# Performance work log

Hardware: AMD Instinct MI355X
Metric: run time of the kernel (lower is better)

Reference implementation:

```python
import jax, jax.numpy as jnp
import numpy as np

ENC_HID = 512
DEC_HID = 512


def setup_inputs() -> dict:
    key = jax.random.key(0)
    k1, k2, k3, k4, k5 = jax.random.split(key, 5)
    hidden = jax.random.normal(k1, (64, DEC_HID), dtype=jnp.float32)
    encoder_outputs = jax.random.normal(k2, (1024, 64, 2 * ENC_HID), dtype=jnp.float32)
    in_dim = 2 * ENC_HID + DEC_HID
    # Linear params (stored as [in, out] for x @ W + b)
    scale = 1.0 / np.sqrt(in_dim)
    W = jax.random.uniform(k3, (in_dim, DEC_HID), dtype=jnp.float32, minval=-scale, maxval=scale)
    b = jax.random.uniform(k4, (DEC_HID,), dtype=jnp.float32, minval=-scale, maxval=scale)
    v = jax.random.uniform(k5, (DEC_HID,), dtype=jnp.float32)  # torch.rand in [0,1)
    return {"hidden": hidden, "encoder_outputs": encoder_outputs, "W": W, "b": b, "v": v}


def reference(hidden, encoder_outputs, W, b, v):
    # hidden: [B, Dd]; encoder_outputs: [S, B, 2*De]
    src_len = encoder_outputs.shape[0]
    enc = jnp.transpose(encoder_outputs, (1, 0, 2))            # [B, S, 2*De]
    hid = jnp.broadcast_to(hidden[:, None, :], (hidden.shape[0], src_len, hidden.shape[1]))  # [B, S, Dd]
    concat = jnp.concatenate([hid, enc], axis=2)               # [B, S, Dd+2*De]
    energy = jnp.tanh(concat @ W + b)                          # [B, S, Dd]
    scores = jnp.einsum("bsd,d->bs", energy, v)                # [B, S]
    return jax.nn.softmax(scores, axis=1)
```

## Files before the change

kernel.cpp:

```cpp
#include <hip/hip_runtime.h>
#include <stdint.h>


typedef float  floatx4 __attribute__((ext_vector_type(4)));
typedef float  floatx8 __attribute__((ext_vector_type(8)));
typedef __bf16 bf16x8  __attribute__((ext_vector_type(8)));
typedef short  short8  __attribute__((ext_vector_type(8)));

union bfu { bf16x8 v; short8 s; };

#define LOG2E_X2 2.8853900817779268f

__device__ __forceinline__ void async_ld16(const void* g, void* l) {
  __builtin_amdgcn_global_load_lds(
      (const __attribute__((address_space(1))) void*)g,
      (__attribute__((address_space(3))) void*)l, 16, 0, 0);
}

__global__ void wt_convert(const float* __restrict__ W, __bf16* __restrict__ Wt) {
  __shared__ float tile[64][65];
  const int kt = blockIdx.x >> 3;
  const int nt = blockIdx.x & 7;
  const int c  = threadIdx.x & 63;
  const int r4 = threadIdx.x >> 6;
  #pragma unroll 4
  for (int i = 0; i < 16; i++) {
    int r = i * 4 + r4;
    tile[r][c] = W[(long)(512 + kt * 64 + r) * 512 + nt * 64 + c];
  }
  __syncthreads();
  #pragma unroll 4
  for (int i = 0; i < 16; i++) {
    int n = i * 4 + r4;
    Wt[(long)(nt * 64 + n) * 1024 + kt * 64 + c] = (__bf16)tile[c][n];
  }
}

__global__ void hproj_kernel(const float* __restrict__ hidden,
                             const float* __restrict__ W,
                             const float* __restrict__ bias,
                             float* __restrict__ hproj) {
  const int tid = threadIdx.x;
  const int b_  = blockIdx.x >> 2;
  const int kc  = blockIdx.x & 3;
  __shared__ float hid[128];
  if (tid < 128) hid[tid] = hidden[b_ * 512 + kc * 128 + tid];
  __syncthreads();
  float acc = (kc == 0) ? bias[tid] : 0.f;
  const float* Wp = W + (long)(kc * 128) * 512 + tid;
  #pragma unroll 8
  for (int k = 0; k < 128; k++) acc = fmaf(hid[k], Wp[(long)k * 512], acc);
  atomicAdd(&hproj[b_ * 512 + tid], acc);
}

__global__ __launch_bounds__(256, 2) void gemm_score(
    const float* __restrict__ enc,
    const __bf16* __restrict__ Wt,
    const float* __restrict__ hproj,
    const float* __restrict__ v,
    float* __restrict__ scores)
{
  __shared__ float ldsA0[2048];
  __shared__ float ldsA1[2048];
  __shared__ float bscore[64];

  const int tid  = threadIdx.x;
  const int lane = tid & 63;
  const int wv   = tid >> 6;
  const int q    = lane >> 4;
  const int t    = lane & 15;
  const long m0  = (long)blockIdx.x * 64;

  const __bf16* bp = Wt + (long)(wv * 128 + t) * 1024 + q * 8;

  if (tid < 64) bscore[tid] = 0.f;

  floatx4 acc[4][8];
  #pragma unroll
  for (int i = 0; i < 4; i++)
    #pragma unroll
    for (int j = 0; j < 8; j++)
      acc[i][j] = (floatx4){0.f, 0.f, 0.f, 0.f};

  auto issueA = [&](int kk, float* buf) {
    #pragma unroll
    for (int i = 0; i < 2; i++) {
      int idx = i * 256 + tid;
      int c = idx >> 7, m = (idx >> 1) & 63, h = idx & 1;
      async_ld16(enc + (m0 + m) * 1024 + kk + c * 8 + h * 4, buf + idx * 4);
    }
  };
  auto loadB = [&](int kk, short8* br) {
    #pragma unroll
    for (int ct = 0; ct < 8; ct++) {
      union bfu u;
      u.v = *(const bf16x8*)(bp + kk + ct * 16 * 1024);
      br[ct] = u.s;
    }
  };
  auto fragA = [&](const float* buf, short8* af) {
    #pragma unroll
    for (int rt = 0; rt < 4; rt++) {
      floatx8 av = *(const floatx8*)(buf + (q * 128 + (rt * 16 + t) * 2) * 4);
      union bfu u;
      #pragma unroll
      for (int j = 0; j < 8; j++) u.v[j] = (__bf16)av[j];
      af[rt] = u.s;
    }
  };
  auto domfma = [&](short8* af, short8* br) {
    #pragma unroll
    for (int rt = 0; rt < 4; rt++)
      #pragma unroll
      for (int ct = 0; ct < 8; ct++)
        acc[rt][ct] = __builtin_amdgcn_mfma_f32_16x16x32_bf16(
            af[rt], br[ct], acc[rt][ct], 0, 0, 0);
  };

  short8 b0[8], b1[8], afr[4];

  issueA(0, ldsA0);
  loadB(0, b0);
  __syncthreads();

  for (int T = 0; T < 16; T++) {
    const int kk = T * 64;
    issueA(kk + 32, ldsA1);
    loadB(kk + 32, b1);
    fragA(ldsA0, afr);
    domfma(afr, b0);
    __syncthreads();

    if (T < 15) {
      issueA(kk + 64, ldsA0);
      loadB(kk + 64, b0);
    }
    fragA(ldsA1, afr);
    domfma(afr, b1);
    __syncthreads();
  }

  float vv[8];
  #pragma unroll
  for (int ct = 0; ct < 8; ct++) vv[ct] = v[wv * 128 + ct * 16 + t];

  #pragma unroll
  for (int rt = 0; rt < 4; rt++) {
    #pragma unroll
    for (int r = 0; r < 4; r++) {
      int row = rt * 16 + q * 4 + r;
      const float* hrow = hproj + row * 512 + wv * 128 + t;
      float s = 0.f;
      #pragma unroll
      for (int ct = 0; ct < 8; ct++) {
        float e  = acc[rt][ct][r] + hrow[ct * 16];
        float ex = __builtin_amdgcn_exp2f(e * LOG2E_X2);
        float th = 1.f - 2.f * __builtin_amdgcn_rcpf(ex + 1.f);
        s = fmaf(vv[ct], th, s);
      }
      s += __shfl_xor(s, 1);
      s += __shfl_xor(s, 2);
      s += __shfl_xor(s, 4);
      s += __shfl_xor(s, 8);
      if (t == 0) atomicAdd(&bscore[row], s);
    }
  }
  __syncthreads();
  if (tid < 64) scores[(long)tid * 1024 + blockIdx.x] = bscore[tid];
}

__global__ void softmax_kernel(const float* __restrict__ scores,
                               float* __restrict__ out) {
  const int b_   = blockIdx.x;
  const int tid  = threadIdx.x;
  const int lane = tid & 63;
  const int wv   = tid >> 6;
  __shared__ float redmax[4], redsum[4];

  float x[4];
  #pragma unroll
  for (int i = 0; i < 4; i++) x[i] = scores[b_ * 1024 + i * 256 + tid];
  float mx = fmaxf(fmaxf(x[0], x[1]), fmaxf(x[2], x[3]));
  #pragma unroll
  for (int off = 1; off < 64; off <<= 1) mx = fmaxf(mx, __shfl_xor(mx, off));
  if (lane == 0) redmax[wv] = mx;
  __syncthreads();
  mx = fmaxf(fmaxf(redmax[0], redmax[1]), fmaxf(redmax[2], redmax[3]));

  float e[4], s = 0.f;
  #pragma unroll
  for (int i = 0; i < 4; i++) { e[i] = __expf(x[i] - mx); s += e[i]; }
  #pragma unroll
  for (int off = 1; off < 64; off <<= 1) s += __shfl_xor(s, off);
  if (lane == 0) redsum[wv] = s;
  __syncthreads();
  s = redsum[0] + redsum[1] + redsum[2] + redsum[3];
  float inv = 1.f / s;
  #pragma unroll
  for (int i = 0; i < 4; i++) out[b_ * 1024 + i * 256 + tid] = e[i] * inv;
}

extern "C" void kernel_launch(void* const* d_in, const int* in_sizes, int n_in,
                              void* d_out, int out_size, void* d_ws, size_t ws_size,
                              hipStream_t stream) {
  (void)in_sizes; (void)n_in; (void)out_size; (void)ws_size;
  const float* hidden = (const float*)d_in[0];
  const float* enc    = (const float*)d_in[1];
  const float* W      = (const float*)d_in[2];
  const float* bias   = (const float*)d_in[3];
  const float* v      = (const float*)d_in[4];
  float* out = (float*)d_out;

  char* ws = (char*)d_ws;
  __bf16* Wt    = (__bf16*)ws;
  float*  hproj = (float*)(ws + (1 << 20));
  float*  scores= (float*)(ws + (1 << 20) + (128 << 10));

  hipMemsetAsync(hproj, 0, 64 * 512 * sizeof(float), stream);
  wt_convert<<<128, 256, 0, stream>>>(W, Wt);
  hproj_kernel<<<256, 512, 0, stream>>>(hidden, W, bias, hproj);
  gemm_score<<<1024, 256, 0, stream>>>(enc, Wt, hproj, v, scores);
  softmax_kernel<<<64, 256, 0, stream>>>(scores, out);
}
```

Measured before the change: 493.0 us.

## Stage encoder tiles through registers as bf16 with deeper software pipeline

```diff
diff --git a/kernel.cpp b/kernel.cpp
--- a/kernel.cpp
+++ b/kernel.cpp
@@ -3,19 +3,12 @@
 
 
 typedef float  floatx4 __attribute__((ext_vector_type(4)));
-typedef float  floatx8 __attribute__((ext_vector_type(8)));
 typedef __bf16 bf16x8  __attribute__((ext_vector_type(8)));
 typedef short  short8  __attribute__((ext_vector_type(8)));
 
 union bfu { bf16x8 v; short8 s; };
 
 #define LOG2E_X2 2.8853900817779268f
-
-__device__ __forceinline__ void async_ld16(const void* g, void* l) {
-  __builtin_amdgcn_global_load_lds(
-      (const __attribute__((address_space(1))) void*)g,
-      (__attribute__((address_space(3))) void*)l, 16, 0, 0);
-}
 
 __global__ void wt_convert(const float* __restrict__ W, __bf16* __restrict__ Wt) {
   __shared__ float tile[64][65];
@@ -60,8 +53,7 @@
     const float* __restrict__ v,
     float* __restrict__ scores)
 {
-  __shared__ float ldsA0[2048];
-  __shared__ float ldsA1[2048];
+  __shared__ __bf16 ldsA[2][2048];
   __shared__ float bscore[64];
 
   const int tid  = threadIdx.x;
@@ -71,6 +63,15 @@
   const int t    = lane & 15;
   const long m0  = (long)blockIdx.x * 64;
 
+  const int sm = tid >> 2;
+  const int sf = tid & 3;
+  const float* ap = enc + (m0 + sm) * 1024 + sf * 8;
+  __bf16* aw0 = &ldsA[0][sf * 512 + sm * 8];
+  __bf16* aw1 = &ldsA[1][sf * 512 + sm * 8];
+
+  const __bf16* ar0 = &ldsA[0][q * 512 + t * 8];
+  const __bf16* ar1 = &ldsA[1][q * 512 + t * 8];
+
   const __bf16* bp = Wt + (long)(wv * 128 + t) * 1024 + q * 8;
 
   if (tid < 64) bscore[tid] = 0.f;
@@ -82,63 +83,66 @@
     for (int j = 0; j < 8; j++)
       acc[i][j] = (floatx4){0.f, 0.f, 0.f, 0.f};
 
-  auto issueA = [&](int kk, float* buf) {
-    #pragma unroll
-    for (int i = 0; i < 2; i++) {
-      int idx = i * 256 + tid;
-      int c = idx >> 7, m = (idx >> 1) & 63, h = idx & 1;
-      async_ld16(enc + (m0 + m) * 1024 + kk + c * 8 + h * 4, buf + idx * 4);
-    }
-  };
-  auto loadB = [&](int kk, short8* br) {
+  floatx4 ra[3][2];
+  short8  bfr[2][8];
+
+  auto issueA = [&](int T, int s) {
+    const float* p = ap + T * 32;
+    ra[s][0] = *(const floatx4*)(p);
+    ra[s][1] = *(const floatx4*)(p + 4);
+  };
+  auto writeA = [&](int s, __bf16* dst) {
+    union bfu u;
+    #pragma unroll
+    for (int j = 0; j < 4; j++) {
+      u.v[j]     = (__bf16)ra[s][0][j];
+      u.v[4 + j] = (__bf16)ra[s][1][j];
+    }
+    *(bf16x8*)dst = u.v;
+  };
+  auto loadB = [&](int T, int s) {
     #pragma unroll
     for (int ct = 0; ct < 8; ct++) {
       union bfu u;
-      u.v = *(const bf16x8*)(bp + kk + ct * 16 * 1024);
-      br[ct] = u.s;
-    }
-  };
-  auto fragA = [&](const float* buf, short8* af) {
+      u.v = *(const bf16x8*)(bp + T * 32 + (long)ct * 16 * 1024);
+      bfr[s][ct] = u.s;
+    }
+  };
+  auto compute = [&](const __bf16* base, int bs) {
     #pragma unroll
     for (int rt = 0; rt < 4; rt++) {
-      floatx8 av = *(const floatx8*)(buf + (q * 128 + (rt * 16 + t) * 2) * 4);
       union bfu u;
-      #pragma unroll
-      for (int j = 0; j < 8; j++) u.v[j] = (__bf16)av[j];
-      af[rt] = u.s;
-    }
-  };
-  auto domfma = [&](short8* af, short8* br) {
-    #pragma unroll
-    for (int rt = 0; rt < 4; rt++)
+      u.v = *(const bf16x8*)(base + rt * 128);
       #pragma unroll
       for (int ct = 0; ct < 8; ct++)
         acc[rt][ct] = __builtin_amdgcn_mfma_f32_16x16x32_bf16(
-            af[rt], br[ct], acc[rt][ct], 0, 0, 0);
-  };
-
-  short8 b0[8], b1[8], afr[4];
-
-  issueA(0, ldsA0);
-  loadB(0, b0);
-  __syncthreads();
-
-  for (int T = 0; T < 16; T++) {
-    const int kk = T * 64;
-    issueA(kk + 32, ldsA1);
-    loadB(kk + 32, b1);
-    fragA(ldsA0, afr);
-    domfma(afr, b0);
-    __syncthreads();
-
-    if (T < 15) {
-      issueA(kk + 64, ldsA0);
-      loadB(kk + 64, b0);
-    }
-    fragA(ldsA1, afr);
-    domfma(afr, b1);
-    __syncthreads();
-  }
+            u.s, bfr[bs][ct], acc[rt][ct], 0, 0, 0);
+    }
+  };
+
+  issueA(0, 0); issueA(1, 1); issueA(2, 2);
+  loadB(0, 0);  loadB(1, 1);
+  writeA(0, aw0);
+  __syncthreads();
+
+#define PHASE(T, SI, SW)                                   \
+  {                                                        \
+    if ((T) < 29) issueA((T) + 3, SI);                     \
+    if ((T) < 31) writeA(SW, ((T) & 1) ? aw0 : aw1);       \
+    compute(((T) & 1) ? ar1 : ar0, (T) & 1);               \
+    if ((T) < 30) loadB((T) + 2, (T) & 1);                 \
+    __syncthreads();                                       \
+  }
+
+  PHASE(0, 0, 1)  PHASE(1, 1, 2)  PHASE(2, 2, 0)  PHASE(3, 0, 1)
+  PHASE(4, 1, 2)  PHASE(5, 2, 0)  PHASE(6, 0, 1)  PHASE(7, 1, 2)
+  PHASE(8, 2, 0)  PHASE(9, 0, 1)  PHASE(10, 1, 2) PHASE(11, 2, 0)
+  PHASE(12, 0, 1) PHASE(13, 1, 2) PHASE(14, 2, 0) PHASE(15, 0, 1)
+  PHASE(16, 1, 2) PHASE(17, 2, 0) PHASE(18, 0, 1) PHASE(19, 1, 2)
+  PHASE(20, 2, 0) PHASE(21, 0, 1) PHASE(22, 1, 2) PHASE(23, 2, 0)
+  PHASE(24, 0, 1) PHASE(25, 1, 2) PHASE(26, 2, 0) PHASE(27, 0, 1)
+  PHASE(28, 1, 2) PHASE(29, 2, 0) PHASE(30, 0, 1) PHASE(31, 1, 2)
+#undef PHASE
 
   float vv[8];
   #pragma unroll
```

Result: no change. 493.2 us (+0.0%).
